# Optimization experiments

Measured on AMD Instinct MI355X. Metric: run time of the kernel, lower is better.

## Reference

```python
import jax, jax.numpy as jnp
import numpy as np

N = 20000
E = 320000
CIN = 16
COUT = 16
D = 4
RADIUS = 0.5


def setup_inputs() -> dict:
    key = jax.random.key(0)
    k1, k2, k3, k4 = jax.random.split(key, 4)
    positions = jax.random.uniform(k1, (N, 3), dtype=jnp.float32)
    features = jax.random.normal(k2, (N, CIN), dtype=jnp.float32)
    filters = jax.random.normal(k3, (D, D, D, CIN, COUT), dtype=jnp.float32)
    edge_index = jax.random.randint(k4, (2, E), 0, N, dtype=jnp.int32)
    return {"positions": positions, "features": features,
            "filters": filters, "edge_index": edge_index}


def _trilinear(filters, gc):
    # Replicates torch grid_sample(align_corners=True) semantics used by the
    # module: grid coord (x,y,z) indexes spatial dims (W,H,D), i.e. gc[:,0]
    # samples filter axis 2, gc[:,1] axis 1, gc[:,2] axis 0.
    Dres = filters.shape[0]
    a, b, c = gc[:, 2], gc[:, 1], gc[:, 0]  # axes 0, 1, 2 of filters
    a0f, b0f, c0f = jnp.floor(a), jnp.floor(b), jnp.floor(c)
    a0 = jnp.clip(a0f.astype(jnp.int32), 0, Dres - 1)
    b0 = jnp.clip(b0f.astype(jnp.int32), 0, Dres - 1)
    c0 = jnp.clip(c0f.astype(jnp.int32), 0, Dres - 1)
    a1 = jnp.minimum(a0 + 1, Dres - 1)
    b1 = jnp.minimum(b0 + 1, Dres - 1)
    c1 = jnp.minimum(c0 + 1, Dres - 1)
    ad = (a - a0f)[:, None, None]  # (E,1,1)
    bd = (b - b0f)[:, None, None]
    cd = (c - c0f)[:, None, None]

    g = lambda i, j, k: filters[i, j, k]  # (E, CIN, COUT) gather
    f00 = g(a0, b0, c0) * (1 - cd) + g(a0, b0, c1) * cd
    f01 = g(a0, b1, c0) * (1 - cd) + g(a0, b1, c1) * cd
    f10 = g(a1, b0, c0) * (1 - cd) + g(a1, b0, c1) * cd
    f11 = g(a1, b1, c0) * (1 - cd) + g(a1, b1, c1) * cd
    f0 = f00 * (1 - bd) + f01 * bd
    f1 = f10 * (1 - bd) + f11 * bd
    return f0 * (1 - ad) + f1 * ad  # (E, CIN, COUT)


def reference(positions, features, filters, edge_index):
    row, col = edge_index[0], edge_index[1]
    r = positions[col] - positions[row]                  # (E,3)
    dist2 = jnp.sum(r * r, axis=-1)                      # (E,)
    valid = (dist2 < RADIUS ** 2).astype(positions.dtype)
    window = (1.0 - dist2 / RADIUS ** 2) ** 3 * valid
    norm = jnp.sqrt(dist2)[:, None]
    mapped = r / (norm + 1e-8) * jnp.tanh(norm)          # ball -> cube, (E,3)
    gc = (mapped + 1.0) * ((filters.shape[0] - 1) / 2.0) # (E,3) in [0, D-1]
    filt = _trilinear(filters, gc)                       # (E, CIN, COUT)
    conv_edge = jnp.einsum('eio,ei->eo', filt, features[col])
    conv_edge = conv_edge * window[:, None]
    n_nodes = positions.shape[0]
    sums = jax.ops.segment_sum(conv_edge, row, num_segments=n_nodes)
    cnt = jax.ops.segment_sum(jnp.ones((conv_edge.shape[0],), positions.dtype),
                              row, num_segments=n_nodes)
    return sums / jnp.maximum(cnt, 1.0)[:, None]         # scatter-mean
```

## Files before the change

kernel.cpp:

```cpp
#include <hip/hip_runtime.h>
#include <hip/hip_fp16.h>
#include <math.h>

#define NN 20000
#define EE 320000
#define CIN 16
#define COUT 16
#define R2C 0.25f
#define MAXDEG 64
#define SLOTC_OFF 81920
#define P_OFF     163840
#define CONV_OFF  (163840 + 40960000)

__global__ __launch_bounds__(256) void k_zero(float* __restrict__ out, int* __restrict__ cnt) {
    int i = blockIdx.x * 256 + threadIdx.x;
    if (i < NN * COUT) out[i] = 0.0f;
    if (i < NN) cnt[i] = 0;
}

__global__ __launch_bounds__(256) void k_pgemm(const float* __restrict__ feat,
                                               const float* __restrict__ filt,
                                               __half* __restrict__ P,
                                               int* __restrict__ cnt_all,
                                               int* __restrict__ slotc) {
    __shared__ float fl[16 * 256];

    if (blockIdx.y == 0) {
        int g = blockIdx.x * 256 + threadIdx.x;
        if (g < NN) { cnt_all[g] = 0; slotc[g] = 0; }
    }

    {
        const float4* src = (const float4*)(filt + (size_t)blockIdx.y * 16 * 256);
        float4* dst = (float4*)fl;
        #pragma unroll
        for (int r = 0; r < 4; ++r)
            dst[r * 256 + threadIdx.x] = src[r * 256 + threadIdx.x];
    }
    __syncthreads();

    int lane  = threadIdx.x & 63;
    int w     = threadIdx.x >> 6;
    int q     = lane & 3;
    int ns    = lane >> 2;
    int nbase = blockIdx.x * 64;

    float f[4][16];
    #pragma unroll
    for (int r = 0; r < 4; ++r) {
        int n = nbase + ns + 16 * r;
        if (n < NN) {
            const float4* fp = (const float4*)(feat + (size_t)n * 16);
            float4 f0 = fp[0], f1 = fp[1], f2 = fp[2], f3 = fp[3];
            f[r][0]=f0.x; f[r][1]=f0.y; f[r][2]=f0.z; f[r][3]=f0.w;
            f[r][4]=f1.x; f[r][5]=f1.y; f[r][6]=f1.z; f[r][7]=f1.w;
            f[r][8]=f2.x; f[r][9]=f2.y; f[r][10]=f2.z; f[r][11]=f2.w;
            f[r][12]=f3.x; f[r][13]=f3.y; f[r][14]=f3.z; f[r][15]=f3.w;
        } else {
            #pragma unroll
            for (int ci = 0; ci < 16; ++ci) f[r][ci] = 0.0f;
        }
    }

    #pragma unroll
    for (int c = 0; c < 4; ++c) {
        int cell = w * 4 + c;
        float4 acc0 = make_float4(0.f,0.f,0.f,0.f);
        float4 acc1 = acc0, acc2 = acc0, acc3 = acc0;
        const float4* row = (const float4*)(fl + cell * 256) + q;
        #pragma unroll
        for (int ci = 0; ci < 16; ++ci) {
            float4 wv = row[ci * 4];
            float v0 = f[0][ci], v1 = f[1][ci], v2 = f[2][ci], v3 = f[3][ci];
            acc0.x = fmaf(v0, wv.x, acc0.x); acc0.y = fmaf(v0, wv.y, acc0.y);
            acc0.z = fmaf(v0, wv.z, acc0.z); acc0.w = fmaf(v0, wv.w, acc0.w);
            acc1.x = fmaf(v1, wv.x, acc1.x); acc1.y = fmaf(v1, wv.y, acc1.y);
            acc1.z = fmaf(v1, wv.z, acc1.z); acc1.w = fmaf(v1, wv.w, acc1.w);
            acc2.x = fmaf(v2, wv.x, acc2.x); acc2.y = fmaf(v2, wv.y, acc2.y);
            acc2.z = fmaf(v2, wv.z, acc2.z); acc2.w = fmaf(v2, wv.w, acc2.w);
            acc3.x = fmaf(v3, wv.x, acc3.x); acc3.y = fmaf(v3, wv.y, acc3.y);
            acc3.z = fmaf(v3, wv.z, acc3.z); acc3.w = fmaf(v3, wv.w, acc3.w);
        }
        size_t cell_g = (size_t)(blockIdx.y * 16 + cell);
        float4 accs[4] = {acc0, acc1, acc2, acc3};
        #pragma unroll
        for (int r = 0; r < 4; ++r) {
            int n = nbase + ns + 16 * r;
            if (n < NN) {
                __half2 lo = __float22half2_rn(make_float2(accs[r].x, accs[r].y));
                __half2 hi = __float22half2_rn(make_float2(accs[r].z, accs[r].w));
                uint2 u;
                u.x = *(unsigned int*)&lo;
                u.y = *(unsigned int*)&hi;
                *(uint2*)(P + (cell_g * NN + n) * 16 + q * 4) = u;
            }
        }
    }
}

__device__ __forceinline__ bool edge_geom(const float* __restrict__ pos, int row, int col,
                                          float& win,
                                          int ia[2], int jb[2], int kc[2],
                                          float wa[2], float wb[2], float wc[2]) {
    float rx = pos[col*3+0] - pos[row*3+0];
    float ry = pos[col*3+1] - pos[row*3+1];
    float rz = pos[col*3+2] - pos[row*3+2];
    float d2 = rx*rx + ry*ry + rz*rz;
    if (!(d2 < R2C)) return false;
    float u = 1.0f - d2 / R2C;
    win = u * u * u;
    float nr = sqrtf(d2);
    float s  = tanhf(nr) / (nr + 1e-8f);
    float gx = (rx * s + 1.0f) * 1.5f;
    float gy = (ry * s + 1.0f) * 1.5f;
    float gz = (rz * s + 1.0f) * 1.5f;
    float af = floorf(gz), bf = floorf(gy), cf = floorf(gx);
    int ia0 = min(max((int)af, 0), 3);
    int ib0 = min(max((int)bf, 0), 3);
    int ic0 = min(max((int)cf, 0), 3);
    ia[0] = ia0; ia[1] = min(ia0 + 1, 3);
    jb[0] = ib0; jb[1] = min(ib0 + 1, 3);
    kc[0] = ic0; kc[1] = min(ic0 + 1, 3);
    float ad = gz - af, bd = gy - bf, cd = gx - cf;
    wa[0] = 1.0f - ad; wa[1] = ad;
    wb[0] = 1.0f - bd; wb[1] = bd;
    wc[0] = 1.0f - cd; wc[1] = cd;
    return true;
}

__global__ __launch_bounds__(256) void k_edge_store(const float* __restrict__ pos,
                                                    const int* __restrict__ ei,
                                                    const __half* __restrict__ P,
                                                    __half* __restrict__ conv,
                                                    int* __restrict__ cnt_all,
                                                    int* __restrict__ slotc) {
    long long t = (long long)blockIdx.x * 256 + threadIdx.x;
    int e = (int)(t >> 3);
    int h = (int)(t & 7);
    if (e >= EE) return;
    int row = ei[e];
    int col = ei[EE + e];
    int lane = threadIdx.x & 63;

    if (h == 0) atomicAdd(&cnt_all[row], 1);

    float win;
    int ia[2], jb[2], kc[2];
    float wa[2], wb[2], wc[2];
    bool valid = edge_geom(pos, row, col, win, ia, jb, kc, wa, wb, wc);

    if (valid) {
        int sv = 0;
        if (h == 0) sv = atomicAdd(&slotc[row], 1);
        int slot = __shfl(sv, lane & 56, 64);

        float2 acc = make_float2(0.f, 0.f);
        const __half* Pq = P + (size_t)col * 16 + h * 2;
        #pragma unroll
        for (int da = 0; da < 2; ++da)
        #pragma unroll
        for (int db = 0; db < 2; ++db)
        #pragma unroll
        for (int dc = 0; dc < 2; ++dc) {
            float w = wa[da] * wb[db] * wc[dc] * win;
            int cell = ia[da]*16 + jb[db]*4 + kc[dc];
            unsigned int raw = *(const unsigned int*)(Pq + (size_t)cell * NN * 16);
            __half2 hv = *(__half2*)&raw;
            float2 p = __half22float2(hv);
            acc.x = fmaf(w, p.x, acc.x);
            acc.y = fmaf(w, p.y, acc.y);
        }
        if (slot < MAXDEG) {
            __half2 hv = __float22half2_rn(acc);
            *(__half2*)(conv + ((size_t)row * MAXDEG + slot) * 16 + h * 2) = hv;
        }
    }
}

__global__ __launch_bounds__(256) void k_gather(const __half* __restrict__ conv,
                                                const int* __restrict__ cnt_all,
                                                const int* __restrict__ slotc,
                                                float* __restrict__ out) {
    int t = blockIdx.x * 256 + threadIdx.x;
    int n = t >> 3;
    int h = t & 7;
    if (n >= NN) return;
    int deg = min(slotc[n], MAXDEG);
    int ca  = cnt_all[n];
    float2 acc = make_float2(0.f, 0.f);
    const __half* base = conv + (size_t)n * MAXDEG * 16 + h * 2;
    for (int s = 0; s < deg; ++s) {
        __half2 hv = *(const __half2*)(base + (size_t)s * 16);
        float2 p = __half22float2(hv);
        acc.x += p.x;
        acc.y += p.y;
    }
    float inv = 1.0f / (float)max(ca, 1);
    float2 r = make_float2(acc.x * inv, acc.y * inv);
    *(float2*)(out + (size_t)n * 16 + h * 2) = r;
}

__global__ __launch_bounds__(256) void k_edge_direct(const float* __restrict__ pos,
                                                     const float* __restrict__ feat,
                                                     const float* __restrict__ filt,
                                                     const int* __restrict__ ei,
                                                     float* __restrict__ out,
                                                     int* __restrict__ cnt) {
    int e = blockIdx.x * 256 + threadIdx.x;
    if (e >= EE) return;
    int row = ei[e];
    int col = ei[EE + e];
    atomicAdd(&cnt[row], 1);

    float win;
    int ia[2], jb[2], kc[2];
    float wa[2], wb[2], wc[2];
    if (!edge_geom(pos, row, col, win, ia, jb, kc, wa, wb, wc)) return;

    float fv[16];
    const float4* fp = (const float4*)(feat + (size_t)col * 16);
    float4 f0 = fp[0], f1 = fp[1], f2 = fp[2], f3 = fp[3];
    fv[0]=f0.x; fv[1]=f0.y; fv[2]=f0.z; fv[3]=f0.w;
    fv[4]=f1.x; fv[5]=f1.y; fv[6]=f1.z; fv[7]=f1.w;
    fv[8]=f2.x; fv[9]=f2.y; fv[10]=f2.z; fv[11]=f2.w;
    fv[12]=f3.x; fv[13]=f3.y; fv[14]=f3.z; fv[15]=f3.w;

    float4 a0 = make_float4(0.f,0.f,0.f,0.f);
    float4 a1 = a0, a2 = a0, a3 = a0;
    for (int da = 0; da < 2; ++da)
    for (int db = 0; db < 2; ++db)
    for (int dc = 0; dc < 2; ++dc) {
        float w = wa[da] * wb[db] * wc[dc] * win;
        const float* fb = filt + (size_t)(ia[da]*16 + jb[db]*4 + kc[dc]) * 256;
        #pragma unroll
        for (int ci = 0; ci < 16; ++ci) {
            float c = w * fv[ci];
            const float4* r4 = (const float4*)(fb + ci * 16);
            float4 w0 = r4[0], w1 = r4[1], w2 = r4[2], w3 = r4[3];
            a0.x = fmaf(c, w0.x, a0.x); a0.y = fmaf(c, w0.y, a0.y);
            a0.z = fmaf(c, w0.z, a0.z); a0.w = fmaf(c, w0.w, a0.w);
            a1.x = fmaf(c, w1.x, a1.x); a1.y = fmaf(c, w1.y, a1.y);
            a1.z = fmaf(c, w1.z, a1.z); a1.w = fmaf(c, w1.w, a1.w);
            a2.x = fmaf(c, w2.x, a2.x); a2.y = fmaf(c, w2.y, a2.y);
            a2.z = fmaf(c, w2.z, a2.z); a2.w = fmaf(c, w2.w, a2.w);
            a3.x = fmaf(c, w3.x, a3.x); a3.y = fmaf(c, w3.y, a3.y);
            a3.z = fmaf(c, w3.z, a3.z); a3.w = fmaf(c, w3.w, a3.w);
        }
    }
    float* op = out + (size_t)row * 16;
    atomicAdd(op+0,  a0.x); atomicAdd(op+1,  a0.y); atomicAdd(op+2,  a0.z); atomicAdd(op+3,  a0.w);
    atomicAdd(op+4,  a1.x); atomicAdd(op+5,  a1.y); atomicAdd(op+6,  a1.z); atomicAdd(op+7,  a1.w);
    atomicAdd(op+8,  a2.x); atomicAdd(op+9,  a2.y); atomicAdd(op+10, a2.z); atomicAdd(op+11, a2.w);
    atomicAdd(op+12, a3.x); atomicAdd(op+13, a3.y); atomicAdd(op+14, a3.z); atomicAdd(op+15, a3.w);
}

__global__ __launch_bounds__(256) void k_div(float* __restrict__ out, const int* __restrict__ cnt) {
    int i = blockIdx.x * 256 + threadIdx.x;
    if (i >= NN * COUT) return;
    int c = cnt[i >> 4];
    float denom = (c > 1) ? (float)c : 1.0f;
    out[i] = out[i] / denom;
}

extern "C" void kernel_launch(void* const* d_in, const int* in_sizes, int n_in,
                              void* d_out, int out_size, void* d_ws, size_t ws_size,
                              hipStream_t stream) {
    const float* pos  = (const float*)d_in[0];
    const float* feat = (const float*)d_in[1];
    const float* filt = (const float*)d_in[2];
    const int*   ei   = (const int*)d_in[3];
    float* out = (float*)d_out;

    int*    cnt_all = (int*)d_ws;
    int*    slotc   = (int*)((char*)d_ws + SLOTC_OFF);
    __half* P       = (__half*)((char*)d_ws + P_OFF);
    __half* conv    = (__half*)((char*)d_ws + CONV_OFF);

    size_t need = (size_t)CONV_OFF + (size_t)NN * MAXDEG * 16 * sizeof(__half);

    if (ws_size >= need) {
        dim3 pg((NN + 63) / 64, 4);
        k_pgemm<<<pg, 256, 0, stream>>>(feat, filt, P, cnt_all, slotc);
        long long tot = (long long)EE * 8;
        k_edge_store<<<(int)((tot + 255) / 256), 256, 0, stream>>>(pos, ei, P, conv, cnt_all, slotc);
        k_gather<<<(NN * 8 + 255) / 256, 256, 0, stream>>>(conv, cnt_all, slotc, out);
    } else {
        k_zero<<<(NN * COUT + 255) / 256, 256, 0, stream>>>(out, cnt_all);
        k_edge_direct<<<(EE + 255) / 256, 256, 0, stream>>>(pos, feat, filt, ei, out, cnt_all);
        k_div<<<(NN * COUT + 255) / 256, 256, 0, stream>>>(out, cnt_all);
    }
}
```

Baseline: 106.5 us.

## Split edge pass into compacted geometry records and dense convolution kernel

Before this, each edge's geometry was computed redundantly by all 8 threads assigned to that edge. Now one thread per edge computes it once and writes a packed 32-byte record (fp16 trilinear weights, cell indices, column, destination slot) into a compacted list of valid edges via an atomic counter. A second kernel launches threads only for valid edges and does the gathers from P. This removes redundant geometry math and idle threads for out-of-radius edges, at the cost of an extra launch, record traffic, a global atomic, and fp16 rounding of the interpolation weights.

```diff
diff --git a/kernel.cpp b/kernel.cpp
--- a/kernel.cpp
+++ b/kernel.cpp
@@ -9,8 +9,10 @@
 #define R2C 0.25f
 #define MAXDEG 64
 #define SLOTC_OFF 81920
+#define NV_OFF    163584
 #define P_OFF     163840
-#define CONV_OFF  (163840 + 40960000)
+#define CONV_OFF  41123840
+#define REC_OFF   82083840
 
 __global__ __launch_bounds__(256) void k_zero(float* __restrict__ out, int* __restrict__ cnt) {
     int i = blockIdx.x * 256 + threadIdx.x;
@@ -22,12 +24,14 @@
                                                const float* __restrict__ filt,
                                                __half* __restrict__ P,
                                                int* __restrict__ cnt_all,
-                                               int* __restrict__ slotc) {
+                                               int* __restrict__ slotc,
+                                               int* __restrict__ nvalid) {
     __shared__ float fl[16 * 256];
 
     if (blockIdx.y == 0) {
         int g = blockIdx.x * 256 + threadIdx.x;
         if (g < NN) { cnt_all[g] = 0; slotc[g] = 0; }
+        if (g == 0) *nvalid = 0;
     }
 
     {
@@ -128,53 +132,89 @@
     return true;
 }
 
-__global__ __launch_bounds__(256) void k_edge_store(const float* __restrict__ pos,
-                                                    const int* __restrict__ ei,
-                                                    const __half* __restrict__ P,
-                                                    __half* __restrict__ conv,
-                                                    int* __restrict__ cnt_all,
-                                                    int* __restrict__ slotc) {
-    long long t = (long long)blockIdx.x * 256 + threadIdx.x;
-    int e = (int)(t >> 3);
-    int h = (int)(t & 7);
+__global__ __launch_bounds__(256) void k_geom(const float* __restrict__ pos,
+                                              const int* __restrict__ ei,
+                                              char* __restrict__ records,
+                                              int* __restrict__ cnt_all,
+                                              int* __restrict__ slotc,
+                                              int* __restrict__ nvalid) {
+    int e = blockIdx.x * 256 + threadIdx.x;
     if (e >= EE) return;
     int row = ei[e];
     int col = ei[EE + e];
-    int lane = threadIdx.x & 63;
-
-    if (h == 0) atomicAdd(&cnt_all[row], 1);
+    atomicAdd(&cnt_all[row], 1);
 
     float win;
     int ia[2], jb[2], kc[2];
     float wa[2], wb[2], wc[2];
-    bool valid = edge_geom(pos, row, col, win, ia, jb, kc, wa, wb, wc);
-
-    if (valid) {
-        int sv = 0;
-        if (h == 0) sv = atomicAdd(&slotc[row], 1);
-        int slot = __shfl(sv, lane & 56, 64);
-
-        float2 acc = make_float2(0.f, 0.f);
-        const __half* Pq = P + (size_t)col * 16 + h * 2;
-        #pragma unroll
-        for (int da = 0; da < 2; ++da)
-        #pragma unroll
-        for (int db = 0; db < 2; ++db)
-        #pragma unroll
-        for (int dc = 0; dc < 2; ++dc) {
-            float w = wa[da] * wb[db] * wc[dc] * win;
-            int cell = ia[da]*16 + jb[db]*4 + kc[dc];
-            unsigned int raw = *(const unsigned int*)(Pq + (size_t)cell * NN * 16);
-            __half2 hv = *(__half2*)&raw;
-            float2 p = __half22float2(hv);
-            acc.x = fmaf(w, p.x, acc.x);
-            acc.y = fmaf(w, p.y, acc.y);
-        }
-        if (slot < MAXDEG) {
-            __half2 hv = __float22half2_rn(acc);
-            *(__half2*)(conv + ((size_t)row * MAXDEG + slot) * 16 + h * 2) = hv;
-        }
-    }
+    if (!edge_geom(pos, row, col, win, ia, jb, kc, wa, wb, wc)) return;
+
+    int slot = atomicAdd(&slotc[row], 1);
+    int vidx = atomicAdd(nvalid, 1);
+
+    float wv[8];
+    unsigned int cc0 = 0, cc1 = 0;
+    #pragma unroll
+    for (int k = 0; k < 8; ++k) {
+        int da = k >> 2, db = (k >> 1) & 1, dc = k & 1;
+        wv[k] = wa[da] * wb[db] * wc[dc] * win;
+        unsigned int cell = (unsigned int)(ia[da]*16 + jb[db]*4 + kc[dc]);
+        if (k < 4) cc0 |= cell << (8 * k);
+        else       cc1 |= cell << (8 * (k - 4));
+    }
+    __half2 w01 = __float22half2_rn(make_float2(wv[0], wv[1]));
+    __half2 w23 = __float22half2_rn(make_float2(wv[2], wv[3]));
+    __half2 w45 = __float22half2_rn(make_float2(wv[4], wv[5]));
+    __half2 w67 = __float22half2_rn(make_float2(wv[6], wv[7]));
+
+    uint4 r0, r1;
+    r0.x = *(unsigned int*)&w01; r0.y = *(unsigned int*)&w23;
+    r0.z = *(unsigned int*)&w45; r0.w = *(unsigned int*)&w67;
+    r1.x = cc0; r1.y = cc1;
+    r1.z = (unsigned int)col;
+    r1.w = (unsigned int)(row * MAXDEG + ((slot < MAXDEG) ? slot : (MAXDEG - 1)));
+
+    uint4* dst = (uint4*)(records + (size_t)vidx * 32);
+    dst[0] = r0; dst[1] = r1;
+}
+
+__global__ __launch_bounds__(256) void k_conv(const char* __restrict__ records,
+                                              const __half* __restrict__ P,
+                                              __half* __restrict__ conv,
+                                              const int* __restrict__ nvalid) {
+    int nv = *nvalid;
+    long long t = (long long)blockIdx.x * 256 + threadIdx.x;
+    int ve = (int)(t >> 3);
+    int h  = (int)(t & 7);
+    if (ve >= nv) return;
+
+    const uint4* rp = (const uint4*)(records + (size_t)ve * 32);
+    uint4 a = rp[0];
+    uint4 b = rp[1];
+
+    float wv[8];
+    {
+        float2 f;
+        f = __half22float2(*(__half2*)&a.x); wv[0] = f.x; wv[1] = f.y;
+        f = __half22float2(*(__half2*)&a.y); wv[2] = f.x; wv[3] = f.y;
+        f = __half22float2(*(__half2*)&a.z); wv[4] = f.x; wv[5] = f.y;
+        f = __half22float2(*(__half2*)&a.w); wv[6] = f.x; wv[7] = f.y;
+    }
+    int col     = (int)b.z;
+    int rowslot = (int)b.w;
+
+    const __half* Pq = P + (size_t)col * 16 + h * 2;
+    float2 acc = make_float2(0.f, 0.f);
+    #pragma unroll
+    for (int k = 0; k < 8; ++k) {
+        unsigned int cell = ((k < 4 ? b.x : b.y) >> (8 * (k & 3))) & 0xffu;
+        unsigned int raw = *(const unsigned int*)(Pq + (size_t)cell * NN * 16);
+        float2 p = __half22float2(*(__half2*)&raw);
+        acc.x = fmaf(wv[k], p.x, acc.x);
+        acc.y = fmaf(wv[k], p.y, acc.y);
+    }
+    __half2 hv = __float22half2_rn(acc);
+    *(__half2*)(conv + (size_t)rowslot * 16 + h * 2) = hv;
 }
 
 __global__ __launch_bounds__(256) void k_gather(const __half* __restrict__ conv,
@@ -273,16 +313,19 @@
 
     int*    cnt_all = (int*)d_ws;
     int*    slotc   = (int*)((char*)d_ws + SLOTC_OFF);
+    int*    nvalid  = (int*)((char*)d_ws + NV_OFF);
     __half* P       = (__half*)((char*)d_ws + P_OFF);
     __half* conv    = (__half*)((char*)d_ws + CONV_OFF);
-
-    size_t need = (size_t)CONV_OFF + (size_t)NN * MAXDEG * 16 * sizeof(__half);
+    char*   records = (char*)d_ws + REC_OFF;
+
+    size_t need = (size_t)REC_OFF + (size_t)EE * 32;
 
     if (ws_size >= need) {
         dim3 pg((NN + 63) / 64, 4);
-        k_pgemm<<<pg, 256, 0, stream>>>(feat, filt, P, cnt_all, slotc);
+        k_pgemm<<<pg, 256, 0, stream>>>(feat, filt, P, cnt_all, slotc, nvalid);
+        k_geom<<<(EE + 255) / 256, 256, 0, stream>>>(pos, ei, records, cnt_all, slotc, nvalid);
         long long tot = (long long)EE * 8;
-        k_edge_store<<<(int)((tot + 255) / 256), 256, 0, stream>>>(pos, ei, P, conv, cnt_all, slotc);
+        k_conv<<<(int)((tot + 255) / 256), 256, 0, stream>>>(records, P, conv, nvalid);
         k_gather<<<(NN * 8 + 255) / 256, 256, 0, stream>>>(conv, cnt_all, slotc, out);
     } else {
         k_zero<<<(NN * COUT + 255) / 256, 256, 0, stream>>>(out, cnt_all);
```

New measurement: 162.1 us. 1.52x slower.
